# Optimization experiments

Measured on AMD Instinct MI355X. Metric: run time of the kernel, lower is better.

The kernel has to match this reference:

```python
import jax, jax.numpy as jnp
import numpy as np


def setup_inputs() -> dict:
    key = jax.random.key(0)
    k1, k2, k3, k4 = jax.random.split(key, 4)
    in_f, out_f, rank, tokens = 4096, 4096, 256, 8192
    bound = 1.0 / np.sqrt(in_f)
    x = jax.random.normal(k1, (tokens, in_f), dtype=jnp.float32)
    U = jax.random.uniform(k2, (out_f, rank), dtype=jnp.float32, minval=-bound, maxval=bound)
    V = jax.random.uniform(k3, (rank, in_f), dtype=jnp.float32, minval=-bound, maxval=bound)
    bias = jax.random.uniform(k4, (out_f,), dtype=jnp.float32, minval=-bound, maxval=bound)
    return {"x": x, "U": U, "V": V, "bias": bias}


def reference(x, U, V, bias):
    # Faithful to original: materialize W = U @ V, then F.linear(x, W, bias) = x @ W.T + bias
    W = U @ V                      # [out, in]
    return x @ W.T + bias          # [tokens, out]
```

## Files before the change

kernel.cpp:

```cpp
#include <hip/hip_runtime.h>
#include <stdint.h>

#define TOKENS 8192
#define INF    4096
#define OUTF   4096
#define RANK   256

typedef __attribute__((ext_vector_type(8))) short bf16x8;
typedef __attribute__((ext_vector_type(4))) float f32x4;

__device__ __forceinline__ unsigned short f2bf(float f) {
    union { float f; unsigned int u; } v; v.f = f;
    unsigned int r = v.u + 0x7FFFu + ((v.u >> 16) & 1u);
    return (unsigned short)(r >> 16);
}

__device__ __forceinline__ void gl_lds16(const void* g, void* l) {
    __builtin_amdgcn_global_load_lds(
        (const __attribute__((address_space(1))) unsigned int*)g,
        (__attribute__((address_space(3))) unsigned int*)l, 16, 0, 0);
}

__global__ void cvt4(const float4* __restrict__ va, ushort4* __restrict__ oa, int na,
                     const float4* __restrict__ vb, ushort4* __restrict__ ob) {
    int i = blockIdx.x * blockDim.x + threadIdx.x;
    float4 v;
    if (i < na) v = va[i]; else v = vb[i - na];
    ushort4 o;
    o.x = f2bf(v.x); o.y = f2bf(v.y); o.z = f2bf(v.z); o.w = f2bf(v.w);
    if (i < na) oa[i] = o; else ob[i - na] = o;
}

#define BM   32
#define BK   128
#define ASTR 136

#define VB0 0
#define VB1 32768
#define AB0 65536
#define AB1 (65536 + 4352)
#define TB0 65536
#define SMSZ 74240

__device__ __forceinline__ void stageV(const unsigned short* __restrict__ Vb,
                                       unsigned short* vdst, int kk,
                                       int wid, int lane) {
    #pragma unroll
    for (int j = 0; j < 8; ++j) {
        int r0  = wid * 32 + j * 4;
        int row = r0 + (lane >> 4);
        int c   = (lane & 15) ^ (row & 7);
        gl_lds16(Vb + (size_t)row * INF + kk + c * 8, vdst + r0 * BK);
    }
}

__device__ __forceinline__ void stageU(const unsigned short* __restrict__ Ub,
                                       unsigned short* udst, int nb,
                                       int wid, int lane) {
    int rp = lane >> 5;
    int c  = lane & 31;
    #pragma unroll
    for (int j = 0; j < 8; ++j) {
        int r0  = wid * 16 + j * 2;
        int row = r0 + rp;
        int sc  = c ^ (row & 7);
        gl_lds16(Ub + (size_t)(nb + row) * RANK + sc * 8, udst + r0 * RANK);
    }
}

__device__ __forceinline__ void g1_pack(float4 a, float4 b, unsigned short* dst) {
    union { bf16x8 v; unsigned short s[8]; } pk;
    pk.s[0] = f2bf(a.x); pk.s[1] = f2bf(a.y);
    pk.s[2] = f2bf(a.z); pk.s[3] = f2bf(a.w);
    pk.s[4] = f2bf(b.x); pk.s[5] = f2bf(b.y);
    pk.s[6] = f2bf(b.z); pk.s[7] = f2bf(b.w);
    *(bf16x8*)dst = pk.v;
}

__device__ __forceinline__ void g1_compute(f32x4 (&acc)[2][2],
                                           const unsigned short* vbuf,
                                           const unsigned short* abuf,
                                           int l15, int quad, int wid) {
    const int rr0 = wid * 32 + l15;
    const int sw  = l15 & 7;
    #pragma unroll
    for (int ks = 0; ks < 4; ++ks) {
        int p = ((ks * 4 + quad) ^ sw) * 8;
        bf16x8 v0 = *(const bf16x8*)&vbuf[rr0 * BK + p];
        bf16x8 v1 = *(const bf16x8*)&vbuf[(rr0 + 16) * BK + p];
        bf16x8 b0 = *(const bf16x8*)&abuf[l15 * ASTR + ks * 32 + quad * 8];
        bf16x8 b1 = *(const bf16x8*)&abuf[(16 + l15) * ASTR + ks * 32 + quad * 8];
        acc[0][0] = __builtin_amdgcn_mfma_f32_16x16x32_bf16(v0, b0, acc[0][0], 0, 0, 0);
        acc[0][1] = __builtin_amdgcn_mfma_f32_16x16x32_bf16(v0, b1, acc[0][1], 0, 0, 0);
        acc[1][0] = __builtin_amdgcn_mfma_f32_16x16x32_bf16(v1, b0, acc[1][0], 0, 0, 0);
        acc[1][1] = __builtin_amdgcn_mfma_f32_16x16x32_bf16(v1, b1, acc[1][1], 0, 0, 0);
    }
}

__device__ __forceinline__ void p2_body(const bf16x8 (&tf)[8][2],
                                        const unsigned short* ubuf,
                                        float* __restrict__ out,
                                        const float* __restrict__ bias,
                                        int m0, int nb, int wid, int l15, int quad) {
    f32x4 a0 = (f32x4){0.f, 0.f, 0.f, 0.f};
    f32x4 a1 = (f32x4){0.f, 0.f, 0.f, 0.f};
    const int ub = (wid * 16 + l15) * RANK;
    const int sw = l15 & 7;
    #pragma unroll
    for (int ks = 0; ks < 8; ++ks) {
        bf16x8 uf = *(const bf16x8*)&ubuf[ub + (((ks * 4 + quad) ^ sw) * 8)];
        a0 = __builtin_amdgcn_mfma_f32_16x16x32_bf16(uf, tf[ks][0], a0, 0, 0, 0);
        a1 = __builtin_amdgcn_mfma_f32_16x16x32_bf16(uf, tf[ks][1], a1, 0, 0, 0);
    }
    const int nc = nb + wid * 16 + quad * 4;
    float4 bb = *(const float4*)&bias[nc];
    float4 v0, v1;
    v0.x = a0[0] + bb.x; v0.y = a0[1] + bb.y; v0.z = a0[2] + bb.z; v0.w = a0[3] + bb.w;
    v1.x = a1[0] + bb.x; v1.y = a1[1] + bb.y; v1.z = a1[2] + bb.z; v1.w = a1[3] + bb.w;
    *(float4*)&out[(size_t)(m0 + l15) * OUTF + nc] = v0;
    *(float4*)&out[(size_t)(m0 + 16 + l15) * OUTF + nc] = v1;
}

__global__ __launch_bounds__(512, 2) void fused(const float* __restrict__ x,
                                                const unsigned short* __restrict__ Vb,
                                                const unsigned short* __restrict__ Ub,
                                                const float* __restrict__ bias,
                                                float* __restrict__ out) {
    __shared__ __align__(16) unsigned short SM[SMSZ];

    const int tid  = threadIdx.x;
    const int lane = tid & 63;
    const int wid  = tid >> 6;
    const int m0   = blockIdx.x * BM;
    const int l15  = lane & 15;
    const int quad = lane >> 4;

    const int arow = tid >> 4;
    const int aseg = tid & 15;
    const float* xp = x + (size_t)(m0 + arow) * INF + aseg * 8;
    unsigned short* aw0 = &SM[AB0 + arow * ASTR + aseg * 8];
    unsigned short* aw1 = &SM[AB1 + arow * ASTR + aseg * 8];

    f32x4 acc[2][2];
    #pragma unroll
    for (int i = 0; i < 2; ++i)
        #pragma unroll
        for (int j = 0; j < 2; ++j) acc[i][j] = (f32x4){0.f, 0.f, 0.f, 0.f};

    stageV(Vb, SM + VB0, 0, wid, lane);
    float4 pA0 = *(const float4*)(xp);
    float4 pA1 = *(const float4*)(xp + 4);
    g1_pack(pA0, pA1, aw0);
    pA0 = *(const float4*)(xp + BK);
    pA1 = *(const float4*)(xp + BK + 4);
    float4 pB0, pB1;

    #pragma unroll 1
    for (int t = 0; t < 30; t += 2) {
        __syncthreads();
        pB0 = *(const float4*)(xp + (t + 2) * BK);
        pB1 = *(const float4*)(xp + (t + 2) * BK + 4);
        stageV(Vb, SM + VB1, (t + 1) * BK, wid, lane);
        g1_compute(acc, SM + VB0, SM + AB0, l15, quad, wid);
        g1_pack(pA0, pA1, aw1);

        __syncthreads();
        pA0 = *(const float4*)(xp + (t + 3) * BK);
        pA1 = *(const float4*)(xp + (t + 3) * BK + 4);
        stageV(Vb, SM + VB0, (t + 2) * BK, wid, lane);
        g1_compute(acc, SM + VB1, SM + AB1, l15, quad, wid);
        g1_pack(pB0, pB1, aw0);
    }
    __syncthreads();
    stageV(Vb, SM + VB1, 31 * BK, wid, lane);
    g1_compute(acc, SM + VB0, SM + AB0, l15, quad, wid);
    g1_pack(pA0, pA1, aw1);
    __syncthreads();
    stageU(Ub, SM + VB0, 0, wid, lane);
    g1_compute(acc, SM + VB1, SM + AB1, l15, quad, wid);
    __syncthreads();

    #pragma unroll
    for (int mv = 0; mv < 2; ++mv)
        #pragma unroll
        for (int mx = 0; mx < 2; ++mx) {
            int tok = mx * 16 + l15;
            int cc  = wid * 4 + mv * 2 + (quad >> 1);
            int sc  = cc ^ (tok & 7);
            ushort4 o;
            o.x = f2bf(acc[mv][mx][0]); o.y = f2bf(acc[mv][mx][1]);
            o.z = f2bf(acc[mv][mx][2]); o.w = f2bf(acc[mv][mx][3]);
            *(ushort4*)&SM[TB0 + tok * RANK + sc * 8 + (quad & 1) * 4] = o;
        }
    __syncthreads();

    bf16x8 tf[8][2];
    #pragma unroll
    for (int ks = 0; ks < 8; ++ks)
        #pragma unroll
        for (int mt = 0; mt < 2; ++mt) {
            int tok = mt * 16 + l15;
            tf[ks][mt] = *(const bf16x8*)
                &SM[TB0 + tok * RANK + (((ks * 4 + quad) ^ (l15 & 7)) * 8)];
        }

    #pragma unroll 1
    for (int u = 0; u < 32; u += 2) {
        if (u) __syncthreads();
        stageU(Ub, SM + VB1, (u + 1) * 128, wid, lane);
        p2_body(tf, SM + VB0, out, bias, m0, u * 128, wid, l15, quad);
        __syncthreads();
        if (u + 2 < 32) stageU(Ub, SM + VB0, (u + 2) * 128, wid, lane);
        p2_body(tf, SM + VB1, out, bias, m0, (u + 1) * 128, wid, l15, quad);
    }
}

extern "C" void kernel_launch(void* const* d_in, const int* in_sizes, int n_in,
                              void* d_out, int out_size, void* d_ws, size_t ws_size,
                              hipStream_t stream) {
    const float* x    = (const float*)d_in[0];
    const float* U    = (const float*)d_in[1];
    const float* V    = (const float*)d_in[2];
    const float* bias = (const float*)d_in[3];
    float* out = (float*)d_out;

    unsigned short* Vb = (unsigned short*)d_ws;
    unsigned short* Ub = Vb + (size_t)RANK * INF;

    const int nv = RANK * INF / 4;
    const int nu = OUTF * RANK / 4;
    cvt4<<<(nv + nu) / 256, 256, 0, stream>>>((const float4*)V, (ushort4*)Vb, nv,
                                              (const float4*)U, (ushort4*)Ub);
    fused<<<TOKENS / BM, 512, 0, stream>>>(x, Vb, Ub, bias, out);
}
```

Baseline: 332.4 us.

## Triple-buffer async LDS pipeline for both GEMM phases with fp32 x staged directly

Restructures the fused low-rank kernel into a three-stage buffer ring with smaller K and N tiles. Both V and x chunks are now loaded straight into LDS with global_load_lds, and stage 2 loads U the same way. Synchronisation uses explicit vmcnt waits plus raw barriers instead of __syncthreads. The fp32 x values are converted to bf16 at fragment-read time with packed v_cvt_pk_bf16_f32, replacing register loads, manual rounding and LDS stores. This aims to overlap global loads with MFMA work and cut register and VALU overhead, but adds more barriers per unit of work and reliance on hand-counted vmcnt.

```diff
diff --git a/kernel.cpp b/kernel.cpp
--- a/kernel.cpp
+++ b/kernel.cpp
@@ -6,13 +6,33 @@
 #define OUTF   4096
 #define RANK   256
 
+#define BM   32
+#define BK   64
+#define BN2  64
+#define NT   64
+
 typedef __attribute__((ext_vector_type(8))) short bf16x8;
 typedef __attribute__((ext_vector_type(4))) float f32x4;
+
+#define VOFF(i) ((i) * 16384)
+#define XOFF(i) (49152 + (i) * 4096)
+#define TOFF    49152
+#define SMSZ    61440
+
+#define WAITV5 asm volatile("s_waitcnt vmcnt(5)" ::: "memory")
+#define WAITV0 asm volatile("s_waitcnt vmcnt(0)" ::: "memory")
+#define BAR    __builtin_amdgcn_s_barrier()
 
 __device__ __forceinline__ unsigned short f2bf(float f) {
     union { float f; unsigned int u; } v; v.f = f;
     unsigned int r = v.u + 0x7FFFu + ((v.u >> 16) & 1u);
     return (unsigned short)(r >> 16);
+}
+
+__device__ __forceinline__ unsigned cvtpk(float lo, float hi) {
+    unsigned r;
+    asm("v_cvt_pk_bf16_f32 %0, %1, %2" : "=v"(r) : "v"(lo), "v"(hi));
+    return r;
 }
 
 __device__ __forceinline__ void gl_lds16(const void* g, void* l) {
@@ -31,95 +51,6 @@
     if (i < na) oa[i] = o; else ob[i - na] = o;
 }
 
-#define BM   32
-#define BK   128
-#define ASTR 136
-
-#define VB0 0
-#define VB1 32768
-#define AB0 65536
-#define AB1 (65536 + 4352)
-#define TB0 65536
-#define SMSZ 74240
-
-__device__ __forceinline__ void stageV(const unsigned short* __restrict__ Vb,
-                                       unsigned short* vdst, int kk,
-                                       int wid, int lane) {
-    #pragma unroll
-    for (int j = 0; j < 8; ++j) {
-        int r0  = wid * 32 + j * 4;
-        int row = r0 + (lane >> 4);
-        int c   = (lane & 15) ^ (row & 7);
-        gl_lds16(Vb + (size_t)row * INF + kk + c * 8, vdst + r0 * BK);
-    }
-}
-
-__device__ __forceinline__ void stageU(const unsigned short* __restrict__ Ub,
-                                       unsigned short* udst, int nb,
-                                       int wid, int lane) {
-    int rp = lane >> 5;
-    int c  = lane & 31;
-    #pragma unroll
-    for (int j = 0; j < 8; ++j) {
-        int r0  = wid * 16 + j * 2;
-        int row = r0 + rp;
-        int sc  = c ^ (row & 7);
-        gl_lds16(Ub + (size_t)(nb + row) * RANK + sc * 8, udst + r0 * RANK);
-    }
-}
-
-__device__ __forceinline__ void g1_pack(float4 a, float4 b, unsigned short* dst) {
-    union { bf16x8 v; unsigned short s[8]; } pk;
-    pk.s[0] = f2bf(a.x); pk.s[1] = f2bf(a.y);
-    pk.s[2] = f2bf(a.z); pk.s[3] = f2bf(a.w);
-    pk.s[4] = f2bf(b.x); pk.s[5] = f2bf(b.y);
-    pk.s[6] = f2bf(b.z); pk.s[7] = f2bf(b.w);
-    *(bf16x8*)dst = pk.v;
-}
-
-__device__ __forceinline__ void g1_compute(f32x4 (&acc)[2][2],
-                                           const unsigned short* vbuf,
-                                           const unsigned short* abuf,
-                                           int l15, int quad, int wid) {
-    const int rr0 = wid * 32 + l15;
-    const int sw  = l15 & 7;
-    #pragma unroll
-    for (int ks = 0; ks < 4; ++ks) {
-        int p = ((ks * 4 + quad) ^ sw) * 8;
-        bf16x8 v0 = *(const bf16x8*)&vbuf[rr0 * BK + p];
-        bf16x8 v1 = *(const bf16x8*)&vbuf[(rr0 + 16) * BK + p];
-        bf16x8 b0 = *(const bf16x8*)&abuf[l15 * ASTR + ks * 32 + quad * 8];
-        bf16x8 b1 = *(const bf16x8*)&abuf[(16 + l15) * ASTR + ks * 32 + quad * 8];
-        acc[0][0] = __builtin_amdgcn_mfma_f32_16x16x32_bf16(v0, b0, acc[0][0], 0, 0, 0);
-        acc[0][1] = __builtin_amdgcn_mfma_f32_16x16x32_bf16(v0, b1, acc[0][1], 0, 0, 0);
-        acc[1][0] = __builtin_amdgcn_mfma_f32_16x16x32_bf16(v1, b0, acc[1][0], 0, 0, 0);
-        acc[1][1] = __builtin_amdgcn_mfma_f32_16x16x32_bf16(v1, b1, acc[1][1], 0, 0, 0);
-    }
-}
-
-__device__ __forceinline__ void p2_body(const bf16x8 (&tf)[8][2],
-                                        const unsigned short* ubuf,
-                                        float* __restrict__ out,
-                                        const float* __restrict__ bias,
-                                        int m0, int nb, int wid, int l15, int quad) {
-    f32x4 a0 = (f32x4){0.f, 0.f, 0.f, 0.f};
-    f32x4 a1 = (f32x4){0.f, 0.f, 0.f, 0.f};
-    const int ub = (wid * 16 + l15) * RANK;
-    const int sw = l15 & 7;
-    #pragma unroll
-    for (int ks = 0; ks < 8; ++ks) {
-        bf16x8 uf = *(const bf16x8*)&ubuf[ub + (((ks * 4 + quad) ^ sw) * 8)];
-        a0 = __builtin_amdgcn_mfma_f32_16x16x32_bf16(uf, tf[ks][0], a0, 0, 0, 0);
-        a1 = __builtin_amdgcn_mfma_f32_16x16x32_bf16(uf, tf[ks][1], a1, 0, 0, 0);
-    }
-    const int nc = nb + wid * 16 + quad * 4;
-    float4 bb = *(const float4*)&bias[nc];
-    float4 v0, v1;
-    v0.x = a0[0] + bb.x; v0.y = a0[1] + bb.y; v0.z = a0[2] + bb.z; v0.w = a0[3] + bb.w;
-    v1.x = a1[0] + bb.x; v1.y = a1[1] + bb.y; v1.z = a1[2] + bb.z; v1.w = a1[3] + bb.w;
-    *(float4*)&out[(size_t)(m0 + l15) * OUTF + nc] = v0;
-    *(float4*)&out[(size_t)(m0 + 16 + l15) * OUTF + nc] = v1;
-}
 
 __global__ __launch_bounds__(512, 2) void fused(const float* __restrict__ x,
                                                 const unsigned short* __restrict__ Vb,
@@ -134,12 +65,14 @@
     const int m0   = blockIdx.x * BM;
     const int l15  = lane & 15;
     const int quad = lane >> 4;
-
-    const int arow = tid >> 4;
-    const int aseg = tid & 15;
-    const float* xp = x + (size_t)(m0 + arow) * INF + aseg * 8;
-    unsigned short* aw0 = &SM[AB0 + arow * ASTR + aseg * 8];
-    unsigned short* aw1 = &SM[AB1 + arow * ASTR + aseg * 8];
+    const int sw8  = l15 & 7;
+
+    const int vrow_j = (lane >> 3);
+    const int vsc    = lane & 7;
+    const int xrow   = wid * 4 + (lane >> 4);
+    const int xsc    = (lane & 15) ^ (xrow & 7);
+    const int urow_j = (lane >> 5);
+    const int usc    = lane & 31;
 
     f32x4 acc[2][2];
     #pragma unroll
@@ -147,71 +80,149 @@
         #pragma unroll
         for (int j = 0; j < 2; ++j) acc[i][j] = (f32x4){0.f, 0.f, 0.f, 0.f};
 
-    stageV(Vb, SM + VB0, 0, wid, lane);
-    float4 pA0 = *(const float4*)(xp);
-    float4 pA1 = *(const float4*)(xp + 4);
-    g1_pack(pA0, pA1, aw0);
-    pA0 = *(const float4*)(xp + BK);
-    pA1 = *(const float4*)(xp + BK + 4);
-    float4 pB0, pB1;
-
-    #pragma unroll 1
-    for (int t = 0; t < 30; t += 2) {
-        __syncthreads();
-        pB0 = *(const float4*)(xp + (t + 2) * BK);
-        pB1 = *(const float4*)(xp + (t + 2) * BK + 4);
-        stageV(Vb, SM + VB1, (t + 1) * BK, wid, lane);
-        g1_compute(acc, SM + VB0, SM + AB0, l15, quad, wid);
-        g1_pack(pA0, pA1, aw1);
-
-        __syncthreads();
-        pA0 = *(const float4*)(xp + (t + 3) * BK);
-        pA1 = *(const float4*)(xp + (t + 3) * BK + 4);
-        stageV(Vb, SM + VB0, (t + 2) * BK, wid, lane);
-        g1_compute(acc, SM + VB1, SM + AB1, l15, quad, wid);
-        g1_pack(pB0, pB1, aw0);
+    auto stageV = [&](int t, int bo) {
+        const int kk = t * BK;
+        #pragma unroll
+        for (int j = 0; j < 4; ++j) {
+            int row = wid * 32 + j * 8 + vrow_j;
+            int c   = vsc ^ (row & 7);
+            gl_lds16(Vb + (size_t)row * INF + kk + c * 8,
+                     &SM[VOFF(bo) + (wid * 32 + j * 8) * BK]);
+        }
+    };
+    auto stageX = [&](int t, int bo) {
+        const int kk = t * BK;
+        gl_lds16(x + (size_t)(m0 + xrow) * INF + kk + xsc * 4,
+                 &SM[XOFF(bo) + wid * 512]);
+    };
+    auto compute1 = [&](int bo) {
+        const unsigned short* vb = &SM[VOFF(bo)];
+        const float* xb = (const float*)&SM[XOFF(bo)];
+        const int rr0 = wid * 32 + l15;
+        #pragma unroll
+        for (int ks = 0; ks < 2; ++ks) {
+            int pv = ((ks * 4 + quad) ^ sw8) * 8;
+            bf16x8 v0 = *(const bf16x8*)&vb[rr0 * BK + pv];
+            bf16x8 v1 = *(const bf16x8*)&vb[(rr0 + 16) * BK + pv];
+            #pragma unroll
+            for (int mt = 0; mt < 2; ++mt) {
+                int tok = mt * 16 + l15;
+                int c0  = ks * 8 + quad * 2;
+                f32x4 lo = *(const f32x4*)&xb[tok * 64 + ((c0    ) ^ sw8) * 4];
+                f32x4 hi = *(const f32x4*)&xb[tok * 64 + ((c0 + 1) ^ sw8) * 4];
+                union { unsigned u[4]; bf16x8 v; } pk;
+                pk.u[0] = cvtpk(lo[0], lo[1]); pk.u[1] = cvtpk(lo[2], lo[3]);
+                pk.u[2] = cvtpk(hi[0], hi[1]); pk.u[3] = cvtpk(hi[2], hi[3]);
+                acc[0][mt] = __builtin_amdgcn_mfma_f32_16x16x32_bf16(v0, pk.v, acc[0][mt], 0, 0, 0);
+                acc[1][mt] = __builtin_amdgcn_mfma_f32_16x16x32_bf16(v1, pk.v, acc[1][mt], 0, 0, 0);
+            }
+        }
+    };
+
+    stageV(0, 0); stageX(0, 0);
+    stageV(1, 1); stageX(1, 1);
+
+    {
+        int cb = 0, sb = 2;
+        #pragma unroll 1
+        for (int t = 0; t < NT - 2; ++t) {
+            WAITV5;
+            BAR;
+            stageV(t + 2, sb); stageX(t + 2, sb);
+            compute1(cb);
+            cb = (cb == 2) ? 0 : cb + 1;
+            sb = (sb == 2) ? 0 : sb + 1;
+        }
+        WAITV5; BAR; compute1(2);
+        WAITV0; BAR; compute1(0);
     }
+
     __syncthreads();
-    stageV(Vb, SM + VB1, 31 * BK, wid, lane);
-    g1_compute(acc, SM + VB0, SM + AB0, l15, quad, wid);
-    g1_pack(pA0, pA1, aw1);
-    __syncthreads();
-    stageU(Ub, SM + VB0, 0, wid, lane);
-    g1_compute(acc, SM + VB1, SM + AB1, l15, quad, wid);
-    __syncthreads();
-
     #pragma unroll
     for (int mv = 0; mv < 2; ++mv)
         #pragma unroll
         for (int mx = 0; mx < 2; ++mx) {
             int tok = mx * 16 + l15;
             int cc  = wid * 4 + mv * 2 + (quad >> 1);
-            int sc  = cc ^ (tok & 7);
-            ushort4 o;
-            o.x = f2bf(acc[mv][mx][0]); o.y = f2bf(acc[mv][mx][1]);
-            o.z = f2bf(acc[mv][mx][2]); o.w = f2bf(acc[mv][mx][3]);
-            *(ushort4*)&SM[TB0 + tok * RANK + sc * 8 + (quad & 1) * 4] = o;
-        }
+            int sc  = cc ^ sw8;
+            union { unsigned u[2]; ushort4 s; } o;
+            o.u[0] = cvtpk(acc[mv][mx][0], acc[mv][mx][1]);
+            o.u[1] = cvtpk(acc[mv][mx][2], acc[mv][mx][3]);
+            *(ushort4*)&SM[TOFF + tok * RANK + sc * 8 + (quad & 1) * 4] = o.s;
+        }
+
+    auto stageU = [&](int t, int bo) {
+        const int nb = t * BN2;
+        #pragma unroll
+        for (int j = 0; j < 4; ++j) {
+            int row = wid * 8 + j * 2 + urow_j;
+            int sc  = usc ^ (row & 7);
+            gl_lds16(Ub + (size_t)(nb + row) * RANK + sc * 8,
+                     &SM[VOFF(bo) + (wid * 8 + j * 2) * RANK]);
+        }
+    };
+    stageU(0, 0); stageU(1, 1);
+
+    const int wy = wid & 1;
+    const int wx = wid >> 1;
+    const int tok2 = wy * 16 + l15;
+    const int biascol = wx * 16 + quad * 4;
+
+    float4 bbA = *(const float4*)&bias[0 * BN2 + biascol];
+    float4 bbB = *(const float4*)&bias[1 * BN2 + biascol];
+
     __syncthreads();
 
-    bf16x8 tf[8][2];
+    bf16x8 tf[8];
     #pragma unroll
     for (int ks = 0; ks < 8; ++ks)
-        #pragma unroll
-        for (int mt = 0; mt < 2; ++mt) {
-            int tok = mt * 16 + l15;
-            tf[ks][mt] = *(const bf16x8*)
-                &SM[TB0 + tok * RANK + (((ks * 4 + quad) ^ (l15 & 7)) * 8)];
-        }
-
-    #pragma unroll 1
-    for (int u = 0; u < 32; u += 2) {
-        if (u) __syncthreads();
-        stageU(Ub, SM + VB1, (u + 1) * 128, wid, lane);
-        p2_body(tf, SM + VB0, out, bias, m0, u * 128, wid, l15, quad);
-        __syncthreads();
-        if (u + 2 < 32) stageU(Ub, SM + VB0, (u + 2) * 128, wid, lane);
-        p2_body(tf, SM + VB1, out, bias, m0, (u + 1) * 128, wid, l15, quad);
+        tf[ks] = *(const bf16x8*)
+            &SM[TOFF + tok2 * RANK + (((ks * 4 + quad) ^ sw8) * 8)];
+
+    const size_t orow = (size_t)(m0 + tok2) * OUTF;
+    const int ur = wx * 16 + l15;
+
+    {
+        int cb = 0, sb = 2;
+        #pragma unroll 1
+        for (int t = 0; t < NT - 1; ++t) {
+            WAITV5;
+            BAR;
+            float4 bnew = make_float4(0.f, 0.f, 0.f, 0.f);
+            if (t + 2 < NT)
+                bnew = *(const float4*)&bias[(t + 2) * BN2 + biascol];
+            if (t + 2 < NT) stageU(t + 2, sb);
+            const unsigned short* ub = &SM[VOFF(cb)];
+            f32x4 a2 = (f32x4){0.f, 0.f, 0.f, 0.f};
+            #pragma unroll
+            for (int ks = 0; ks < 8; ++ks) {
+                bf16x8 uf = *(const bf16x8*)
+                    &ub[ur * RANK + (((ks * 4 + quad) ^ sw8) * 8)];
+                a2 = __builtin_amdgcn_mfma_f32_16x16x32_bf16(uf, tf[ks], a2, 0, 0, 0);
+            }
+            int nc = t * BN2 + biascol;
+            float4 v;
+            v.x = a2[0] + bbA.x; v.y = a2[1] + bbA.y;
+            v.z = a2[2] + bbA.z; v.w = a2[3] + bbA.w;
+            *(float4*)&out[orow + nc] = v;
+            bbA = bbB; bbB = bnew;
+            cb = (cb == 2) ? 0 : cb + 1;
+            sb = (sb == 2) ? 0 : sb + 1;
+        }
+        WAITV0; BAR;
+        const unsigned short* ub = &SM[VOFF(0)];
+        f32x4 a2 = (f32x4){0.f, 0.f, 0.f, 0.f};
+        #pragma unroll
+        for (int ks = 0; ks < 8; ++ks) {
+            bf16x8 uf = *(const bf16x8*)
+                &ub[ur * RANK + (((ks * 4 + quad) ^ sw8) * 8)];
+            a2 = __builtin_amdgcn_mfma_f32_16x16x32_bf16(uf, tf[ks], a2, 0, 0, 0);
+        }
+        int nc = (NT - 1) * BN2 + biascol;
+        float4 v;
+        v.x = a2[0] + bbA.x; v.y = a2[1] + bbA.y;
+        v.z = a2[2] + bbA.z; v.w = a2[3] + bbA.w;
+        *(float4*)&out[orow + nc] = v;
     }
 }
 
```

Result: no change. 336.3 us (+1.2%).
